# Kernel optimization log

Measured on AMD Instinct MI355X. Metric: run time of the kernel, lower is better.

## Reference

```python
import jax, jax.numpy as jnp
import numpy as np

N = 50000      # nodes
E = 800000     # edges (before self-loops)
IN = 128       # in_channels
HID = 16       # hidden_channels
HEADS = 8
OUT = 16       # out_channels
NEG_SLOPE = 0.2
BN_EPS = 1e-5
LN_EPS = 1e-5


def setup_inputs() -> dict:
    key = jax.random.key(0)
    ks = jax.random.split(key, 16)
    s = 0.05
    inp = {
        "x": jax.random.normal(ks[0], (N, IN), jnp.float32),
        "edge_index": jax.random.randint(ks[1], (2, E), 0, N, jnp.int64),
        # conv1 (in=IN, out=HID, heads=HEADS, concat=True)
        "Wl1": jax.random.normal(ks[2], (HEADS * HID, IN), jnp.float32) * s,
        "bl1": jnp.zeros((HEADS * HID,), jnp.float32),
        "Wr1": jax.random.normal(ks[3], (HEADS * HID, IN), jnp.float32) * s,
        "br1": jnp.zeros((HEADS * HID,), jnp.float32),
        "att1": jax.random.normal(ks[4], (HEADS, HID), jnp.float32) * s,
        "bias1": jnp.zeros((HEADS * HID,), jnp.float32),
        # batchnorm (eval mode, running stats)
        "bn_w": jnp.ones((HEADS * HID,), jnp.float32),
        "bn_b": jnp.zeros((HEADS * HID,), jnp.float32),
        "bn_rm": jnp.zeros((HEADS * HID,), jnp.float32),
        "bn_rv": jnp.ones((HEADS * HID,), jnp.float32),
        # conv2 (in=HEADS*HID, out=OUT, heads=HEADS, concat=False)
        "Wl2": jax.random.normal(ks[5], (HEADS * OUT, HEADS * HID), jnp.float32) * s,
        "bl2": jnp.zeros((HEADS * OUT,), jnp.float32),
        "Wr2": jax.random.normal(ks[6], (HEADS * OUT, HEADS * HID), jnp.float32) * s,
        "br2": jnp.zeros((HEADS * OUT,), jnp.float32),
        "att2": jax.random.normal(ks[7], (HEADS, OUT), jnp.float32) * s,
        "bias2": jnp.zeros((OUT,), jnp.float32),
        # skip + layernorm
        "Wskip": jax.random.normal(ks[8], (OUT, IN), jnp.float32) * s,
        "ln_w": jnp.ones((OUT,), jnp.float32),
        "ln_b": jnp.zeros((OUT,), jnp.float32),
    }
    return inp


def _gatv2(x, src, dst, Wl, bl, Wr, br, att, bias, heads, ch, concat):
    """PyG GATv2Conv (share_weights=False), eval mode (no dropout)."""
    n = x.shape[0]
    xl = (x @ Wl.T + bl).reshape(n, heads, ch)   # source transform
    xr = (x @ Wr.T + br).reshape(n, heads, ch)   # target transform
    # edge-wise attention score
    e = jax.nn.leaky_relu(xl[src] + xr[dst], NEG_SLOPE)          # [E',H,C]
    score = jnp.einsum('ehc,hc->eh', e, att)                      # [E',H]
    # segment softmax over incoming edges per destination node
    smax = jax.ops.segment_max(score, dst, num_segments=n)
    ex = jnp.exp(score - smax[dst])
    denom = jax.ops.segment_sum(ex, dst, num_segments=n)
    alpha = ex / denom[dst]                                       # [E',H]
    out = jax.ops.segment_sum(alpha[:, :, None] * xl[src], dst, num_segments=n)
    if concat:
        out = out.reshape(n, heads * ch)
    else:
        out = out.mean(axis=1)
    return out + bias


def reference(x, edge_index, Wl1, bl1, Wr1, br1, att1, bias1,
              bn_w, bn_b, bn_rm, bn_rv,
              Wl2, bl2, Wr2, br2, att2, bias2,
              Wskip, ln_w, ln_b):
    n = x.shape[0]
    loops = jnp.arange(n, dtype=edge_index.dtype)
    src = jnp.concatenate([edge_index[0], loops])
    dst = jnp.concatenate([edge_index[1], loops])

    x_res = x @ Wskip.T                                            # [N,OUT]

    h = _gatv2(x, src, dst, Wl1, bl1, Wr1, br1, att1, bias1, HEADS, HID, True)
    # BatchNorm1d in eval mode
    h = (h - bn_rm) * jax.lax.rsqrt(bn_rv + BN_EPS) * bn_w + bn_b
    h = jax.nn.elu(h)

    h = _gatv2(h, src, dst, Wl2, bl2, Wr2, br2, att2, bias2, HEADS, OUT, False)

    y = h + x_res
    mu = y.mean(axis=-1, keepdims=True)
    var = ((y - mu) ** 2).mean(axis=-1, keepdims=True)
    return (y - mu) * jax.lax.rsqrt(var + LN_EPS) * ln_w + ln_b
```

## Files before the change

kernel.cpp:

```cpp
#include <hip/hip_runtime.h>

#define NEG_SLOPE 0.2f
#define BN_EPS 1e-5f
#define LN_EPS 1e-5f

#if __has_builtin(__builtin_amdgcn_exp2f)
#define EXP2F(x) __builtin_amdgcn_exp2f(x)
#else
#define EXP2F(x) exp2f(x)
#endif

typedef __bf16 bf16_t;
typedef bf16_t bf16x8 __attribute__((ext_vector_type(8)));
typedef float floatx4 __attribute__((ext_vector_type(4)));

__device__ __forceinline__ unsigned short f2bf(float f) {
  unsigned u = __float_as_uint(f);
  u += 0x7FFFu + ((u >> 16) & 1u);
  return (unsigned short)(u >> 16);
}
__device__ __forceinline__ float bf_lo(unsigned u) { return __uint_as_float(u << 16); }
__device__ __forceinline__ float bf_hi(unsigned u) { return __uint_as_float(u & 0xFFFF0000u); }

__global__ void cvt_all(const float* __restrict__ x,
                        const float* __restrict__ wl1, const float* __restrict__ wr1,
                        const float* __restrict__ wl2, const float* __restrict__ wr2,
                        const float* __restrict__ wsk,
                        const float* __restrict__ bias1,
                        const float* __restrict__ bn_w, const float* __restrict__ bn_b,
                        const float* __restrict__ bn_rm, const float* __restrict__ bn_rv,
                        const int* __restrict__ ei, int E,
                        unsigned short* __restrict__ xbf,
                        unsigned short* __restrict__ wcat1,
                        unsigned short* __restrict__ wcat2,
                        int* __restrict__ deg8, unsigned short* __restrict__ rpos,
                        float* __restrict__ bnS, float* __restrict__ bnT,
                        int n4x, int N) {
  const int W4 = 128 * 128 / 4;
  const int S4 = 16 * 128 / 4;
  int i = blockIdx.x * blockDim.x + threadIdx.x;
  const float* src;
  unsigned short* dst;
  int j;
  if (i < n4x) { src = x; dst = xbf; j = i; }
  else {
    j = i - n4x;
    if (j < W4)               { src = wl1; dst = wcat1; }
    else if (j < 2 * W4)      { src = wr1; dst = wcat1 + 128 * 128; j -= W4; }
    else if (j < 3 * W4)      { src = wl2; dst = wcat2; j -= 2 * W4; }
    else if (j < 4 * W4)      { src = wr2; dst = wcat2 + 128 * 128; j -= 3 * W4; }
    else if (j < 4 * W4 + S4) { src = wsk; dst = wcat1 + 256 * 128; j -= 4 * W4; }
    else {
      j -= 4 * W4 + S4;
      if (j < 32) {
        for (int t = j * 4; t < j * 4 + 4; ++t) {
          float S = bn_w[t] * rsqrtf(bn_rv[t] + BN_EPS);
          bnS[t] = S;
          bnT[t] = (bias1[t] - bn_rm[t]) * S + bn_b[t];
        }
      } else {
        int e = j - 32;
        if (e < E) {
          int d = ei[E + e];
          int c = (int)(blockIdx.x & 7);
          rpos[e] = (unsigned short)atomicAdd(&deg8[(size_t)c * N + d], 1);
        }
      }
      return;
    }
  }
  float4 v = ((const float4*)src)[j];
  ushort4 o;
  o.x = f2bf(v.x); o.y = f2bf(v.y); o.z = f2bf(v.z); o.w = f2bf(v.w);
  ((ushort4*)dst)[j] = o;
}

__global__ __launch_bounds__(1024)
void csr_scan(const int* __restrict__ deg8, int* __restrict__ meta,
              int* __restrict__ cbase8, int* bsum, int N) {
  __shared__ int wsum[16];
  __shared__ int sh_base;
  int b = blockIdx.x;
  int tid = threadIdx.x;
  int lane = tid & 63, wid = tid >> 6;
  int i0 = b * 4096 + tid * 4;

  int4 v[8];
#pragma unroll
  for (int c = 0; c < 8; ++c) {
    const int* p = deg8 + (size_t)c * N;
    v[c] = make_int4(0, 0, 0, 0);
    if (i0 + 3 < N) v[c] = *(const int4*)(p + i0);
    else if (i0 < N) {
      v[c].x = p[i0];
      if (i0 + 1 < N) v[c].y = p[i0 + 1];
      if (i0 + 2 < N) v[c].z = p[i0 + 2];
    }
  }
  int4 run = make_int4(0, 0, 0, 0);
#pragma unroll
  for (int c = 0; c < 8; ++c) {
    int4 t = v[c];
    v[c] = run;
    run.x += t.x; run.y += t.y; run.z += t.z; run.w += t.w;
  }
  int g1 = (run.x + 1) & ~1, g2 = (run.y + 1) & ~1, g3 = (run.z + 1) & ~1, g4 = (run.w + 1) & ~1;
  int s1 = g1, s2 = s1 + g2, s3 = s2 + g3, s4 = s3 + g4;
  int s = s4;
#pragma unroll
  for (int d = 1; d < 64; d <<= 1) { int t = __shfl_up(s, d, 64); if (lane >= d) s += t; }
  if (lane == 63) wsum[wid] = s;
  __syncthreads();
  if (tid < 16) {
    int ws = wsum[tid];
#pragma unroll
    for (int d = 1; d < 16; d <<= 1) { int t = __shfl_up(ws, d, 16); if (tid >= d) ws += t; }
    wsum[tid] = ws;
  }
  __syncthreads();
  if (tid == 0) {
    __hip_atomic_store(&bsum[b], wsum[15] + 1, __ATOMIC_RELEASE, __HIP_MEMORY_SCOPE_AGENT);
    int base = 0;
    for (int j = 0; j < b; ++j) {
      int x;
      do { x = __hip_atomic_load(&bsum[j], __ATOMIC_ACQUIRE, __HIP_MEMORY_SCOPE_AGENT); } while (x == 0);
      base += x - 1;
    }
    sh_base = base;
  }
  __syncthreads();
  int off = sh_base + (wid ? wsum[wid - 1] : 0) + (s - s4);
  int st[4] = {off, off + s1, off + s2, off + s3};
  int tv[4] = {run.x, run.y, run.z, run.w};
#pragma unroll
  for (int k = 0; k < 4; ++k)
    if (i0 + k < N) ((int2*)meta)[i0 + k] = make_int2(st[k], tv[k]);
#pragma unroll
  for (int c = 0; c < 8; ++c) {
    int* p = cbase8 + (size_t)c * N;
    if (i0 + 3 < N) {
      *(int4*)(p + i0) = make_int4(st[0] + v[c].x, st[1] + v[c].y, st[2] + v[c].z, st[3] + v[c].w);
    } else if (i0 < N) {
      p[i0] = st[0] + v[c].x;
      if (i0 + 1 < N) p[i0 + 1] = st[1] + v[c].y;
      if (i0 + 2 < N) p[i0 + 2] = st[2] + v[c].z;
    }
  }
}

__global__ void scatter_edges(const int* __restrict__ ei, int E, int ebase,
                              const int* __restrict__ cbase8,
                              const unsigned short* __restrict__ rpos,
                              unsigned short* __restrict__ csr, int N) {
  int e = blockIdx.x * blockDim.x + threadIdx.x;
  if (e < E) {
    int d = ei[E + e];
    int c = ((ebase + e) >> 8) & 7;
    csr[cbase8[(size_t)c * N + d] + (int)rpos[e]] = (unsigned short)ei[e];
  }
}

template <bool MIXED>
__global__ __launch_bounds__(256)
void gemm_bf16_mfma(const unsigned short* __restrict__ A, const unsigned short* __restrict__ B,
                    const float* __restrict__ bias0, const float* __restrict__ bias1,
                    unsigned short* __restrict__ Cbf, float* __restrict__ Cf,
                    int M, int pstrips) {
  int wave = (int)((blockIdx.x * blockDim.x + threadIdx.x) >> 6);
  int lane = threadIdx.x & 63;
  int mtiles = (M + 31) >> 5;
  if (wave >= mtiles * pstrips) return;
  int mt = wave % mtiles, ps = wave / mtiles;
  int r = lane & 15, quad = lane >> 4;

  const unsigned short* Abase = A + (size_t)(mt * 32 + r) * 128 + quad * 8;
  bf16x8 a0[4], a1[4];
#pragma unroll
  for (int k = 0; k < 4; ++k) {
    a0[k] = *(const bf16x8*)(Abase + 32 * k);
    a1[k] = *(const bf16x8*)(Abase + 16 * 128 + 32 * k);
  }

  int row0 = mt * 32 + quad * 4;
  const int Ptot = MIXED ? 272 : 256;
#pragma unroll
  for (int pp = 0; pp < 4; ++pp) {
    int p0 = ps * 64 + pp * 16;
    if (p0 >= Ptot) break;
    const unsigned short* Bbase = B + (size_t)(p0 + r) * 128 + quad * 8;
    bf16x8 b[4];
#pragma unroll
    for (int k = 0; k < 4; ++k) b[k] = *(const bf16x8*)(Bbase + 32 * k);
    floatx4 acc0 = {0.f, 0.f, 0.f, 0.f};
    floatx4 acc1 = {0.f, 0.f, 0.f, 0.f};
#pragma unroll
    for (int k = 0; k < 4; ++k) {
      acc0 = __builtin_amdgcn_mfma_f32_16x16x32_bf16(a0[k], b[k], acc0, 0, 0, 0);
      acc1 = __builtin_amdgcn_mfma_f32_16x16x32_bf16(a1[k], b[k], acc1, 0, 0, 0);
    }
    int col = p0 + r;
    if (MIXED && col >= 256) {
#pragma unroll
      for (int i = 0; i < 4; ++i) {
        if (row0 + i < M)      Cf[(size_t)(row0 + i) * 16 + (col - 256)] = acc0[i];
        if (row0 + 16 + i < M) Cf[(size_t)(row0 + 16 + i) * 16 + (col - 256)] = acc1[i];
      }
    } else {
      float bs = (col < 128) ? bias0[col] : bias1[col - 128];
#pragma unroll
      for (int i = 0; i < 4; ++i) {
        if (row0 + i < M)      Cbf[(size_t)(row0 + i) * 256 + col] = f2bf(acc0[i] + bs);
        if (row0 + 16 + i < M) Cbf[(size_t)(row0 + 16 + i) * 256 + col] = f2bf(acc1[i] + bs);
      }
    }
  }
}

template <int LAYER>
__global__ __launch_bounds__(256)
void gat_agg(const unsigned int* __restrict__ xlr,
             const int* __restrict__ meta,
             const unsigned short* __restrict__ csr,
             const float* __restrict__ att,
             const float* __restrict__ p0, const float* __restrict__ p1,
             const float* __restrict__ p2, const float* __restrict__ p3,
             void* __restrict__ outp, int n, int nwaves) {
  int lane = threadIdx.x & 63;
  int gw = (int)((blockIdx.x * blockDim.x + threadIdx.x) >> 6);
  int half = lane >> 5, sl = lane & 31;
  float4 at = ((const float4*)att)[sl];
  const float SC = 0.6f * 1.44269504f;
  float a0 = SC * at.x, a1 = SC * at.y, a2 = SC * at.z, a3 = SC * at.w;

  for (int dst = gw; dst < n; dst += nwaves) {
    int dsts = __builtin_amdgcn_readfirstlane(dst);
    int2 m = *(const int2*)(meta + 2 * (size_t)dsts);
    int beg = __builtin_amdgcn_readfirstlane(m.x);
    int dg  = __builtin_amdgcn_readfirstlane(m.y);
    const unsigned* cp = (const unsigned*)csr + (beg >> 1);

    uint2 ur = *(const uint2*)(xlr + (size_t)dsts * 128 + 64 + sl * 2);
    float xr0 = bf_lo(ur.x), xr1 = bf_hi(ur.x), xr2 = bf_lo(ur.y), xr3 = bf_hi(ur.y);
    float lA = 0.f, lB = 0.f;
    float cA0 = 0.f, cA1 = 0.f, cA2 = 0.f, cA3 = 0.f;
    float cB0 = 0.f, cB1 = 0.f, cB2 = 0.f, cB3 = 0.f;

    auto body = [&](uint2 u, float vm, bool useB, bool masked) {
      float x0 = bf_lo(u.x), x1 = bf_hi(u.x), x2 = bf_lo(u.y), x3 = bf_hi(u.y);
      float e0 = x0 + xr0, e1 = x1 + xr1, e2 = x2 + xr2, e3 = x3 + xr3;
      float sc = fmaf(fmaf(fabsf(e0), 0.66666667f, e0), a0,
                 fmaf(fmaf(fabsf(e1), 0.66666667f, e1), a1,
                 fmaf(fmaf(fabsf(e2), 0.66666667f, e2), a2,
                      fmaf(fabsf(e3), 0.66666667f, e3) * a3)));
      sc += __shfl_xor(sc, 1);
      sc += __shfl_xor(sc, 2);
      float pw = EXP2F(sc);
      if (masked) pw *= vm;
      if (useB) {
        lB += pw;
        cB0 = fmaf(pw, x0, cB0); cB1 = fmaf(pw, x1, cB1);
        cB2 = fmaf(pw, x2, cB2); cB3 = fmaf(pw, x3, cB3);
      } else {
        lA += pw;
        cA0 = fmaf(pw, x0, cA0); cA1 = fmaf(pw, x1, cA1);
        cA2 = fmaf(pw, x2, cA2); cA3 = fmaf(pw, x3, cA3);
      }
    };

    int npm = dg >> 1;
    int p = 0;
    int npm8 = npm & ~7;
    for (; p < npm8; p += 8) {
      uint2 u[8];
#pragma unroll
      for (int k = 0; k < 8; ++k) {
        unsigned pr = cp[p + k];
        int s = half ? (int)(pr >> 16) : (int)(pr & 0xFFFFu);
        u[k] = *(const uint2*)(xlr + ((size_t)s << 7) + sl * 2);
      }
#pragma unroll
      for (int k = 0; k < 8; ++k) body(u[k], 1.f, k & 1, false);
    }
    if (npm - p >= 4) {
      uint2 u[4];
#pragma unroll
      for (int k = 0; k < 4; ++k) {
        unsigned pr = cp[p + k];
        int s = half ? (int)(pr >> 16) : (int)(pr & 0xFFFFu);
        u[k] = *(const uint2*)(xlr + ((size_t)s << 7) + sl * 2);
      }
#pragma unroll
      for (int k = 0; k < 4; ++k) body(u[k], 1.f, k & 1, false);
      p += 4;
    }
    {
      int tot = dg + 1;
      uint2 u[4];
      float vm[4];
#pragma unroll
      for (int k = 0; k < 4; ++k) {
        unsigned pr = cp[p + k];
        int e0 = 2 * (p + k), e1 = e0 + 1;
        int sA = (e0 < dg) ? (int)(pr & 0xFFFFu) : dsts;
        int sB = (e1 < dg) ? (int)(pr >> 16) : dsts;
        float mA = (e0 < tot) ? 1.f : 0.f;
        float mB = (e1 < tot) ? 1.f : 0.f;
        int s = half ? sB : sA;
        vm[k] = half ? mB : mA;
        u[k] = *(const uint2*)(xlr + ((size_t)s << 7) + sl * 2);
      }
#pragma unroll
      for (int k = 0; k < 4; ++k) body(u[k], vm[k], k & 1, true);
    }

    float l = lA + lB;
    float c0 = cA0 + cB0, c1 = cA1 + cB1, c2 = cA2 + cB2, c3 = cA3 + cB3;
    l  += __shfl_xor(l, 32);
    c0 += __shfl_xor(c0, 32); c1 += __shfl_xor(c1, 32);
    c2 += __shfl_xor(c2, 32); c3 += __shfl_xor(c3, 32);
    float inv = 1.f / l;

    if (LAYER == 1) {
      float4 S = ((const float4*)p0)[sl];
      float4 T = ((const float4*)p1)[sl];
      float o0 = fmaf(c0 * inv, S.x, T.x);
      float o1 = fmaf(c1 * inv, S.y, T.y);
      float o2 = fmaf(c2 * inv, S.z, T.z);
      float o3 = fmaf(c3 * inv, S.w, T.w);
      o0 = (o0 > 0.f) ? o0 : (__expf(o0) - 1.f);
      o1 = (o1 > 0.f) ? o1 : (__expf(o1) - 1.f);
      o2 = (o2 > 0.f) ? o2 : (__expf(o2) - 1.f);
      o3 = (o3 > 0.f) ? o3 : (__expf(o3) - 1.f);
      if (half == 0) {
        uint2 o;
        o.x = ((unsigned)f2bf(o1) << 16) | f2bf(o0);
        o.y = ((unsigned)f2bf(o3) << 16) | f2bf(o2);
        ((uint2*)outp)[(size_t)dst * 32 + sl] = o;
      }
    } else {
      float y0 = c0 * inv, y1 = c1 * inv, y2 = c2 * inv, y3 = c3 * inv;
#pragma unroll
      for (int d = 4; d <= 16; d <<= 1) {
        y0 += __shfl_xor(y0, d); y1 += __shfl_xor(y1, d);
        y2 += __shfl_xor(y2, d); y3 += __shfl_xor(y3, d);
      }
      int chh = (sl & 3) * 4;
      float4 b2 = *(const float4*)(p1 + chh);
      float4 xs = *(const float4*)(p0 + (size_t)dst * 16 + chh);
      y0 = y0 * 0.125f + b2.x + xs.x;
      y1 = y1 * 0.125f + b2.y + xs.y;
      y2 = y2 * 0.125f + b2.z + xs.z;
      y3 = y3 * 0.125f + b2.w + xs.w;
      float t = (y0 + y1) + (y2 + y3);
      t += __shfl_xor(t, 1); t += __shfl_xor(t, 2);
      float mu = t * (1.f / 16.f);
      float d0 = y0 - mu, d1 = y1 - mu, d2 = y2 - mu, d3 = y3 - mu;
      float v = (d0 * d0 + d1 * d1) + (d2 * d2 + d3 * d3);
      v += __shfl_xor(v, 1); v += __shfl_xor(v, 2);
      float istd = rsqrtf(v * (1.f / 16.f) + LN_EPS);
      float4 lw = *(const float4*)(p2 + chh);
      float4 lb = *(const float4*)(p3 + chh);
      if (lane < 4) {
        float4 o;
        o.x = d0 * istd * lw.x + lb.x;
        o.y = d1 * istd * lw.y + lb.y;
        o.z = d2 * istd * lw.z + lb.z;
        o.w = d3 * istd * lw.w + lb.w;
        *(float4*)((float*)outp + (size_t)dst * 16 + chh) = o;
      }
    }
  }
}

extern "C" void kernel_launch(void* const* d_in, const int* in_sizes, int n_in,
                              void* d_out, int out_size, void* d_ws, size_t ws_size,
                              hipStream_t stream) {
  const float* x     = (const float*)d_in[0];
  const int*   ei    = (const int*)d_in[1];
  const float* Wl1   = (const float*)d_in[2];
  const float* bl1   = (const float*)d_in[3];
  const float* Wr1   = (const float*)d_in[4];
  const float* br1   = (const float*)d_in[5];
  const float* att1  = (const float*)d_in[6];
  const float* bias1 = (const float*)d_in[7];
  const float* bn_w  = (const float*)d_in[8];
  const float* bn_b  = (const float*)d_in[9];
  const float* bn_rm = (const float*)d_in[10];
  const float* bn_rv = (const float*)d_in[11];
  const float* Wl2   = (const float*)d_in[12];
  const float* bl2   = (const float*)d_in[13];
  const float* Wr2   = (const float*)d_in[14];
  const float* br2   = (const float*)d_in[15];
  const float* att2  = (const float*)d_in[16];
  const float* bias2 = (const float*)d_in[17];
  const float* Wskip = (const float*)d_in[18];
  const float* ln_w  = (const float*)d_in[19];
  const float* ln_b  = (const float*)d_in[20];

  const int N = in_sizes[0] / 128;
  const int E = in_sizes[1] / 2;

  char* w = (char*)d_ws;
  size_t off = 0;
  auto alloc = [&](size_t bytes) -> void* {
    void* p = (void*)(w + off);
    off += (bytes + 255) & ~(size_t)255;
    return p;
  };
  unsigned short* xbf    = (unsigned short*)alloc((size_t)N * 128 * 2);
  unsigned short* wcat1  = (unsigned short*)alloc(272 * 128 * 2);
  unsigned short* wcat2  = (unsigned short*)alloc(256 * 128 * 2);
  unsigned int*   xlr    = (unsigned int*)alloc((size_t)N * 128 * 4);
  float*          xres   = (float*)alloc((size_t)N * 16 * 4);
  unsigned short* hbf    = (unsigned short*)alloc((size_t)N * 128 * 2);
  float*          bnS    = (float*)alloc(128 * 4);
  float*          bnT    = (float*)alloc(128 * 4);
  int*            deg8   = (int*)alloc((size_t)8 * N * 4);
  int*            bsum   = (int*)alloc(64 * 4);
  int*            cbase8 = (int*)alloc((size_t)8 * N * 4);
  int*            meta   = (int*)alloc((size_t)2 * N * 4);
  unsigned short* rpos   = (unsigned short*)alloc((size_t)E * 2);
  unsigned short* csr    = (unsigned short*)alloc((size_t)(E + N) * 2 + 256);

  const int n4x = (N * 128) / 4;
  const int W4 = 128 * 128 / 4, S4 = 16 * 128 / 4;
  const int ebase = n4x + 4 * W4 + S4 + 32;
  const int nb = (N + 4095) / 4096;

  hipMemsetAsync(deg8, 0, (size_t)8 * N * 4 + 256 + 64 * 4, stream);
  {
    int tot = ebase + E;
    cvt_all<<<(tot + 255) / 256, 256, 0, stream>>>(
        x, Wl1, Wr1, Wl2, Wr2, Wskip, bias1, bn_w, bn_b, bn_rm, bn_rv, ei, E,
        xbf, wcat1, wcat2, deg8, rpos, bnS, bnT, n4x, N);
  }

  csr_scan<<<nb, 1024, 0, stream>>>(deg8, meta, cbase8, bsum, N);
  scatter_edges<<<(E + 255) / 256, 256, 0, stream>>>(ei, E, ebase, cbase8, rpos, csr, N);

  {
    int mtiles = (N + 31) >> 5;
    int waves = mtiles * 5;
    gemm_bf16_mfma<true><<<(waves + 3) / 4, 256, 0, stream>>>(
        xbf, wcat1, bl1, br1, (unsigned short*)xlr, xres, N, 5);
  }

  {
    int blocks = 2048, nwaves = blocks * 4;
    gat_agg<1><<<blocks, 256, 0, stream>>>(xlr, meta, csr, att1,
                                           bnS, bnT, nullptr, nullptr, (void*)hbf, N, nwaves);
  }

  {
    int mtiles = (N + 31) >> 5;
    int waves = mtiles * 4;
    gemm_bf16_mfma<false><<<(waves + 3) / 4, 256, 0, stream>>>(
        hbf, wcat2, bl2, br2, (unsigned short*)xlr, nullptr, N, 4);
  }

  {
    int blocks = 2048, nwaves = blocks * 4;
    gat_agg<2><<<blocks, 256, 0, stream>>>(xlr, meta, csr, att2,
                                           xres, bias2, ln_w, ln_b, d_out, N, nwaves);
  }
}
```

Measured before the change: 302.8 us.

## Reuse A fragments across strips in GEMM and prefetch next node metadata in aggregation

```diff
diff --git a/kernel.cpp b/kernel.cpp
--- a/kernel.cpp
+++ b/kernel.cpp
@@ -166,11 +166,11 @@
                     const float* __restrict__ bias0, const float* __restrict__ bias1,
                     unsigned short* __restrict__ Cbf, float* __restrict__ Cf,
                     int M, int pstrips) {
-  int wave = (int)((blockIdx.x * blockDim.x + threadIdx.x) >> 6);
+  int wv = (int)((blockIdx.x * blockDim.x + threadIdx.x) >> 6);
   int lane = threadIdx.x & 63;
   int mtiles = (M + 31) >> 5;
-  if (wave >= mtiles * pstrips) return;
-  int mt = wave % mtiles, ps = wave / mtiles;
+  if (wv >= mtiles * 2) return;
+  int mt = wv >> 1, sub = wv & 1;
   int r = lane & 15, quad = lane >> 4;
 
   const unsigned short* Abase = A + (size_t)(mt * 32 + r) * 128 + quad * 8;
@@ -183,34 +183,36 @@
 
   int row0 = mt * 32 + quad * 4;
   const int Ptot = MIXED ? 272 : 256;
-#pragma unroll
-  for (int pp = 0; pp < 4; ++pp) {
-    int p0 = ps * 64 + pp * 16;
-    if (p0 >= Ptot) break;
-    const unsigned short* Bbase = B + (size_t)(p0 + r) * 128 + quad * 8;
-    bf16x8 b[4];
-#pragma unroll
-    for (int k = 0; k < 4; ++k) b[k] = *(const bf16x8*)(Bbase + 32 * k);
-    floatx4 acc0 = {0.f, 0.f, 0.f, 0.f};
-    floatx4 acc1 = {0.f, 0.f, 0.f, 0.f};
-#pragma unroll
-    for (int k = 0; k < 4; ++k) {
-      acc0 = __builtin_amdgcn_mfma_f32_16x16x32_bf16(a0[k], b[k], acc0, 0, 0, 0);
-      acc1 = __builtin_amdgcn_mfma_f32_16x16x32_bf16(a1[k], b[k], acc1, 0, 0, 0);
-    }
-    int col = p0 + r;
-    if (MIXED && col >= 256) {
-#pragma unroll
-      for (int i = 0; i < 4; ++i) {
-        if (row0 + i < M)      Cf[(size_t)(row0 + i) * 16 + (col - 256)] = acc0[i];
-        if (row0 + 16 + i < M) Cf[(size_t)(row0 + 16 + i) * 16 + (col - 256)] = acc1[i];
-      }
-    } else {
-      float bs = (col < 128) ? bias0[col] : bias1[col - 128];
-#pragma unroll
-      for (int i = 0; i < 4; ++i) {
-        if (row0 + i < M)      Cbf[(size_t)(row0 + i) * 256 + col] = f2bf(acc0[i] + bs);
-        if (row0 + 16 + i < M) Cbf[(size_t)(row0 + 16 + i) * 256 + col] = f2bf(acc1[i] + bs);
+  for (int ps = sub; ps < pstrips; ps += 2) {
+#pragma unroll
+    for (int pp = 0; pp < 4; ++pp) {
+      int p0 = ps * 64 + pp * 16;
+      if (p0 >= Ptot) break;
+      const unsigned short* Bbase = B + (size_t)(p0 + r) * 128 + quad * 8;
+      bf16x8 b[4];
+#pragma unroll
+      for (int k = 0; k < 4; ++k) b[k] = *(const bf16x8*)(Bbase + 32 * k);
+      floatx4 acc0 = {0.f, 0.f, 0.f, 0.f};
+      floatx4 acc1 = {0.f, 0.f, 0.f, 0.f};
+#pragma unroll
+      for (int k = 0; k < 4; ++k) {
+        acc0 = __builtin_amdgcn_mfma_f32_16x16x32_bf16(a0[k], b[k], acc0, 0, 0, 0);
+        acc1 = __builtin_amdgcn_mfma_f32_16x16x32_bf16(a1[k], b[k], acc1, 0, 0, 0);
+      }
+      int col = p0 + r;
+      if (MIXED && col >= 256) {
+#pragma unroll
+        for (int i = 0; i < 4; ++i) {
+          if (row0 + i < M)      Cf[(size_t)(row0 + i) * 16 + (col - 256)] = acc0[i];
+          if (row0 + 16 + i < M) Cf[(size_t)(row0 + 16 + i) * 16 + (col - 256)] = acc1[i];
+        }
+      } else {
+        float bs = (col < 128) ? bias0[col] : bias1[col - 128];
+#pragma unroll
+        for (int i = 0; i < 4; ++i) {
+          if (row0 + i < M)      Cbf[(size_t)(row0 + i) * 256 + col] = f2bf(acc0[i] + bs);
+          if (row0 + 16 + i < M) Cbf[(size_t)(row0 + 16 + i) * 256 + col] = f2bf(acc1[i] + bs);
+        }
       }
     }
   }
@@ -228,22 +230,47 @@
   int lane = threadIdx.x & 63;
   int gw = (int)((blockIdx.x * blockDim.x + threadIdx.x) >> 6);
   int half = lane >> 5, sl = lane & 31;
+  const char* __restrict__ xb = (const char*)xlr;
+  const unsigned slOff = (unsigned)(sl << 3);
+  const int hshift = half << 4;
   float4 at = ((const float4*)att)[sl];
   const float SC = 0.6f * 1.44269504f;
   float a0 = SC * at.x, a1 = SC * at.y, a2 = SC * at.z, a3 = SC * at.w;
 
-  for (int dst = gw; dst < n; dst += nwaves) {
+  int dst = gw;
+  int2 m = make_int2(0, 0);
+  uint2 ur = make_uint2(0u, 0u);
+  if (dst < n) {
+    int ds0 = __builtin_amdgcn_readfirstlane(dst);
+    m = *(const int2*)(meta + 2 * (size_t)ds0);
+    ur = *(const uint2*)(xb + (((unsigned)ds0 << 9) + 256u + slOff));
+  }
+
+  while (dst < n) {
     int dsts = __builtin_amdgcn_readfirstlane(dst);
-    int2 m = *(const int2*)(meta + 2 * (size_t)dsts);
     int beg = __builtin_amdgcn_readfirstlane(m.x);
     int dg  = __builtin_amdgcn_readfirstlane(m.y);
     const unsigned* cp = (const unsigned*)csr + (beg >> 1);
 
-    uint2 ur = *(const uint2*)(xlr + (size_t)dsts * 128 + 64 + sl * 2);
     float xr0 = bf_lo(ur.x), xr1 = bf_hi(ur.x), xr2 = bf_lo(ur.y), xr3 = bf_hi(ur.y);
+
+    int nxt = dst + nwaves;
+    int2 m_n = make_int2(0, 0);
+    uint2 ur_n = make_uint2(0u, 0u);
+    if (nxt < n) {
+      int dsn = __builtin_amdgcn_readfirstlane(nxt);
+      m_n = *(const int2*)(meta + 2 * (size_t)dsn);
+      ur_n = *(const uint2*)(xb + (((unsigned)dsn << 9) + 256u + slOff));
+    }
+
     float lA = 0.f, lB = 0.f;
     float cA0 = 0.f, cA1 = 0.f, cA2 = 0.f, cA3 = 0.f;
     float cB0 = 0.f, cB1 = 0.f, cB2 = 0.f, cB3 = 0.f;
+
+    auto gat = [&](unsigned pr) -> uint2 {
+      unsigned s = (pr >> hshift) & 0xFFFFu;
+      return *(const uint2*)(xb + ((s << 9) + slOff));
+    };
 
     auto body = [&](uint2 u, float vm, bool useB, bool masked) {
       float x0 = bf_lo(u.x), x1 = bf_hi(u.x), x2 = bf_lo(u.y), x3 = bf_hi(u.y);
@@ -273,44 +300,56 @@
     for (; p < npm8; p += 8) {
       uint2 u[8];
 #pragma unroll
-      for (int k = 0; k < 8; ++k) {
-        unsigned pr = cp[p + k];
-        int s = half ? (int)(pr >> 16) : (int)(pr & 0xFFFFu);
-        u[k] = *(const uint2*)(xlr + ((size_t)s << 7) + sl * 2);
-      }
+      for (int k = 0; k < 8; ++k) u[k] = gat(cp[p + k]);
 #pragma unroll
       for (int k = 0; k < 8; ++k) body(u[k], 1.f, k & 1, false);
     }
     if (npm - p >= 4) {
       uint2 u[4];
 #pragma unroll
-      for (int k = 0; k < 4; ++k) {
-        unsigned pr = cp[p + k];
-        int s = half ? (int)(pr >> 16) : (int)(pr & 0xFFFFu);
-        u[k] = *(const uint2*)(xlr + ((size_t)s << 7) + sl * 2);
-      }
+      for (int k = 0; k < 4; ++k) u[k] = gat(cp[p + k]);
 #pragma unroll
       for (int k = 0; k < 4; ++k) body(u[k], 1.f, k & 1, false);
       p += 4;
     }
     {
       int tot = dg + 1;
-      uint2 u[4];
-      float vm[4];
-#pragma unroll
-      for (int k = 0; k < 4; ++k) {
-        unsigned pr = cp[p + k];
-        int e0 = 2 * (p + k), e1 = e0 + 1;
-        int sA = (e0 < dg) ? (int)(pr & 0xFFFFu) : dsts;
-        int sB = (e1 < dg) ? (int)(pr >> 16) : dsts;
-        float mA = (e0 < tot) ? 1.f : 0.f;
-        float mB = (e1 < tot) ? 1.f : 0.f;
-        int s = half ? sB : sA;
-        vm[k] = half ? mB : mA;
-        u[k] = *(const uint2*)(xlr + ((size_t)s << 7) + sl * 2);
-      }
-#pragma unroll
-      for (int k = 0; k < 4; ++k) body(u[k], vm[k], k & 1, true);
+      int need = tot - 2 * p;
+      if (need > 4) {
+        uint2 u[4];
+        float vm[4];
+#pragma unroll
+        for (int k = 0; k < 4; ++k) {
+          unsigned pr = cp[p + k];
+          int e0 = 2 * (p + k), e1 = e0 + 1;
+          int sA = (e0 < dg) ? (int)(pr & 0xFFFFu) : dsts;
+          int sB = (e1 < dg) ? (int)(pr >> 16) : dsts;
+          float mA = (e0 < tot) ? 1.f : 0.f;
+          float mB = (e1 < tot) ? 1.f : 0.f;
+          unsigned s = (unsigned)(half ? sB : sA);
+          vm[k] = half ? mB : mA;
+          u[k] = *(const uint2*)(xb + ((s << 9) + slOff));
+        }
+#pragma unroll
+        for (int k = 0; k < 4; ++k) body(u[k], vm[k], k & 1, true);
+      } else {
+        uint2 u[2];
+        float vm[2];
+#pragma unroll
+        for (int k = 0; k < 2; ++k) {
+          unsigned pr = cp[p + k];
+          int e0 = 2 * (p + k), e1 = e0 + 1;
+          int sA = (e0 < dg) ? (int)(pr & 0xFFFFu) : dsts;
+          int sB = (e1 < dg) ? (int)(pr >> 16) : dsts;
+          float mA = (e0 < tot) ? 1.f : 0.f;
+          float mB = (e1 < tot) ? 1.f : 0.f;
+          unsigned s = (unsigned)(half ? sB : sA);
+          vm[k] = half ? mB : mA;
+          u[k] = *(const uint2*)(xb + ((s << 9) + slOff));
+        }
+#pragma unroll
+        for (int k = 0; k < 2; ++k) body(u[k], vm[k], k & 1, true);
+      }
     }
 
     float l = lA + lB;
@@ -369,6 +408,10 @@
         *(float4*)((float*)outp + (size_t)dst * 16 + chh) = o;
       }
     }
+
+    m = m_n;
+    ur = ur_n;
+    dst = nxt;
   }
 }
 
@@ -440,7 +483,7 @@
 
   {
     int mtiles = (N + 31) >> 5;
-    int waves = mtiles * 5;
+    int waves = mtiles * 2;
     gemm_bf16_mfma<true><<<(waves + 3) / 4, 256, 0, stream>>>(
         xbf, wcat1, bl1, br1, (unsigned short*)xlr, xres, N, 5);
   }
@@ -453,7 +496,7 @@
 
   {
     int mtiles = (N + 31) >> 5;
-    int waves = mtiles * 4;
+    int waves = mtiles * 2;
     gemm_bf16_mfma<false><<<(waves + 3) / 4, 256, 0, stream>>>(
         hbf, wcat2, bl2, br2, (unsigned short*)xlr, nullptr, N, 4);
   }
```

Result: no change. 306.1 us (+1.1%).

## Add atomic work-stealing scheduler to GAT aggregation and reuse A tiles across GEMM strips

Applied to the files above, without the earlier changes.

```diff
diff --git a/kernel.cpp b/kernel.cpp
--- a/kernel.cpp
+++ b/kernel.cpp
@@ -166,11 +166,11 @@
                     const float* __restrict__ bias0, const float* __restrict__ bias1,
                     unsigned short* __restrict__ Cbf, float* __restrict__ Cf,
                     int M, int pstrips) {
-  int wave = (int)((blockIdx.x * blockDim.x + threadIdx.x) >> 6);
+  int wv = (int)((blockIdx.x * blockDim.x + threadIdx.x) >> 6);
   int lane = threadIdx.x & 63;
   int mtiles = (M + 31) >> 5;
-  if (wave >= mtiles * pstrips) return;
-  int mt = wave % mtiles, ps = wave / mtiles;
+  if (wv >= mtiles * 2) return;
+  int mt = wv >> 1, sub = wv & 1;
   int r = lane & 15, quad = lane >> 4;
 
   const unsigned short* Abase = A + (size_t)(mt * 32 + r) * 128 + quad * 8;
@@ -183,34 +183,36 @@
 
   int row0 = mt * 32 + quad * 4;
   const int Ptot = MIXED ? 272 : 256;
-#pragma unroll
-  for (int pp = 0; pp < 4; ++pp) {
-    int p0 = ps * 64 + pp * 16;
-    if (p0 >= Ptot) break;
-    const unsigned short* Bbase = B + (size_t)(p0 + r) * 128 + quad * 8;
-    bf16x8 b[4];
-#pragma unroll
-    for (int k = 0; k < 4; ++k) b[k] = *(const bf16x8*)(Bbase + 32 * k);
-    floatx4 acc0 = {0.f, 0.f, 0.f, 0.f};
-    floatx4 acc1 = {0.f, 0.f, 0.f, 0.f};
-#pragma unroll
-    for (int k = 0; k < 4; ++k) {
-      acc0 = __builtin_amdgcn_mfma_f32_16x16x32_bf16(a0[k], b[k], acc0, 0, 0, 0);
-      acc1 = __builtin_amdgcn_mfma_f32_16x16x32_bf16(a1[k], b[k], acc1, 0, 0, 0);
-    }
-    int col = p0 + r;
-    if (MIXED && col >= 256) {
-#pragma unroll
-      for (int i = 0; i < 4; ++i) {
-        if (row0 + i < M)      Cf[(size_t)(row0 + i) * 16 + (col - 256)] = acc0[i];
-        if (row0 + 16 + i < M) Cf[(size_t)(row0 + 16 + i) * 16 + (col - 256)] = acc1[i];
-      }
-    } else {
-      float bs = (col < 128) ? bias0[col] : bias1[col - 128];
-#pragma unroll
-      for (int i = 0; i < 4; ++i) {
-        if (row0 + i < M)      Cbf[(size_t)(row0 + i) * 256 + col] = f2bf(acc0[i] + bs);
-        if (row0 + 16 + i < M) Cbf[(size_t)(row0 + 16 + i) * 256 + col] = f2bf(acc1[i] + bs);
+  for (int ps = sub; ps < pstrips; ps += 2) {
+#pragma unroll
+    for (int pp = 0; pp < 4; ++pp) {
+      int p0 = ps * 64 + pp * 16;
+      if (p0 >= Ptot) break;
+      const unsigned short* Bbase = B + (size_t)(p0 + r) * 128 + quad * 8;
+      bf16x8 b[4];
+#pragma unroll
+      for (int k = 0; k < 4; ++k) b[k] = *(const bf16x8*)(Bbase + 32 * k);
+      floatx4 acc0 = {0.f, 0.f, 0.f, 0.f};
+      floatx4 acc1 = {0.f, 0.f, 0.f, 0.f};
+#pragma unroll
+      for (int k = 0; k < 4; ++k) {
+        acc0 = __builtin_amdgcn_mfma_f32_16x16x32_bf16(a0[k], b[k], acc0, 0, 0, 0);
+        acc1 = __builtin_amdgcn_mfma_f32_16x16x32_bf16(a1[k], b[k], acc1, 0, 0, 0);
+      }
+      int col = p0 + r;
+      if (MIXED && col >= 256) {
+#pragma unroll
+        for (int i = 0; i < 4; ++i) {
+          if (row0 + i < M)      Cf[(size_t)(row0 + i) * 16 + (col - 256)] = acc0[i];
+          if (row0 + 16 + i < M) Cf[(size_t)(row0 + 16 + i) * 16 + (col - 256)] = acc1[i];
+        }
+      } else {
+        float bs = (col < 128) ? bias0[col] : bias1[col - 128];
+#pragma unroll
+        for (int i = 0; i < 4; ++i) {
+          if (row0 + i < M)      Cbf[(size_t)(row0 + i) * 256 + col] = f2bf(acc0[i] + bs);
+          if (row0 + 16 + i < M) Cbf[(size_t)(row0 + 16 + i) * 256 + col] = f2bf(acc1[i] + bs);
+        }
       }
     }
   }
@@ -224,26 +226,40 @@
              const float* __restrict__ att,
              const float* __restrict__ p0, const float* __restrict__ p1,
              const float* __restrict__ p2, const float* __restrict__ p3,
-             void* __restrict__ outp, int n, int nwaves) {
+             void* __restrict__ outp, int n,
+             int* __restrict__ cursor, int pp) {
   int lane = threadIdx.x & 63;
-  int gw = (int)((blockIdx.x * blockDim.x + threadIdx.x) >> 6);
   int half = lane >> 5, sl = lane & 31;
+  const char* __restrict__ xb = (const char*)xlr;
+  const unsigned slOff = (unsigned)(sl << 3);
+  const int hshift = half << 4;
   float4 at = ((const float4*)att)[sl];
   const float SC = 0.6f * 1.44269504f;
   float a0 = SC * at.x, a1 = SC * at.y, a2 = SC * at.z, a3 = SC * at.w;
 
-  for (int dst = gw; dst < n; dst += nwaves) {
-    int dsts = __builtin_amdgcn_readfirstlane(dst);
+  const int g = (int)(blockIdx.x & 7);
+  const int base = g * pp;
+  const int lim = min(pp, n - base);
+  const int wig = (int)(blockIdx.x >> 3) * (int)(blockDim.x >> 6) + (int)(threadIdx.x >> 6);
+  const int seed = (int)(gridDim.x >> 3) * (int)(blockDim.x >> 6) * 4;
+
+  auto process = [&](int dstv) {
+    int dsts = __builtin_amdgcn_readfirstlane(dstv);
     int2 m = *(const int2*)(meta + 2 * (size_t)dsts);
     int beg = __builtin_amdgcn_readfirstlane(m.x);
     int dg  = __builtin_amdgcn_readfirstlane(m.y);
     const unsigned* cp = (const unsigned*)csr + (beg >> 1);
-
-    uint2 ur = *(const uint2*)(xlr + (size_t)dsts * 128 + 64 + sl * 2);
+    uint2 ur = *(const uint2*)(xb + (((unsigned)dsts << 9) + 256u + slOff));
     float xr0 = bf_lo(ur.x), xr1 = bf_hi(ur.x), xr2 = bf_lo(ur.y), xr3 = bf_hi(ur.y);
+
     float lA = 0.f, lB = 0.f;
     float cA0 = 0.f, cA1 = 0.f, cA2 = 0.f, cA3 = 0.f;
     float cB0 = 0.f, cB1 = 0.f, cB2 = 0.f, cB3 = 0.f;
+
+    auto gat = [&](unsigned pr) -> uint2 {
+      unsigned s = (pr >> hshift) & 0xFFFFu;
+      return *(const uint2*)(xb + ((s << 9) + slOff));
+    };
 
     auto body = [&](uint2 u, float vm, bool useB, bool masked) {
       float x0 = bf_lo(u.x), x1 = bf_hi(u.x), x2 = bf_lo(u.y), x3 = bf_hi(u.y);
@@ -273,22 +289,14 @@
     for (; p < npm8; p += 8) {
       uint2 u[8];
 #pragma unroll
-      for (int k = 0; k < 8; ++k) {
-        unsigned pr = cp[p + k];
-        int s = half ? (int)(pr >> 16) : (int)(pr & 0xFFFFu);
-        u[k] = *(const uint2*)(xlr + ((size_t)s << 7) + sl * 2);
-      }
+      for (int k = 0; k < 8; ++k) u[k] = gat(cp[p + k]);
 #pragma unroll
       for (int k = 0; k < 8; ++k) body(u[k], 1.f, k & 1, false);
     }
     if (npm - p >= 4) {
       uint2 u[4];
 #pragma unroll
-      for (int k = 0; k < 4; ++k) {
-        unsigned pr = cp[p + k];
-        int s = half ? (int)(pr >> 16) : (int)(pr & 0xFFFFu);
-        u[k] = *(const uint2*)(xlr + ((size_t)s << 7) + sl * 2);
-      }
+      for (int k = 0; k < 4; ++k) u[k] = gat(cp[p + k]);
 #pragma unroll
       for (int k = 0; k < 4; ++k) body(u[k], 1.f, k & 1, false);
       p += 4;
@@ -305,9 +313,9 @@
         int sB = (e1 < dg) ? (int)(pr >> 16) : dsts;
         float mA = (e0 < tot) ? 1.f : 0.f;
         float mB = (e1 < tot) ? 1.f : 0.f;
-        int s = half ? sB : sA;
+        unsigned s = (unsigned)(half ? sB : sA);
         vm[k] = half ? mB : mA;
-        u[k] = *(const uint2*)(xlr + ((size_t)s << 7) + sl * 2);
+        u[k] = *(const uint2*)(xb + ((s << 9) + slOff));
       }
 #pragma unroll
       for (int k = 0; k < 4; ++k) body(u[k], vm[k], k & 1, true);
@@ -335,7 +343,7 @@
         uint2 o;
         o.x = ((unsigned)f2bf(o1) << 16) | f2bf(o0);
         o.y = ((unsigned)f2bf(o3) << 16) | f2bf(o2);
-        ((uint2*)outp)[(size_t)dst * 32 + sl] = o;
+        ((uint2*)outp)[(size_t)dsts * 32 + sl] = o;
       }
     } else {
       float y0 = c0 * inv, y1 = c1 * inv, y2 = c2 * inv, y3 = c3 * inv;
@@ -346,7 +354,7 @@
       }
       int chh = (sl & 3) * 4;
       float4 b2 = *(const float4*)(p1 + chh);
-      float4 xs = *(const float4*)(p0 + (size_t)dst * 16 + chh);
+      float4 xs = *(const float4*)(p0 + (size_t)dsts * 16 + chh);
       y0 = y0 * 0.125f + b2.x + xs.x;
       y1 = y1 * 0.125f + b2.y + xs.y;
       y2 = y2 * 0.125f + b2.z + xs.z;
@@ -366,9 +374,24 @@
         o.y = d1 * istd * lw.y + lb.y;
         o.z = d2 * istd * lw.z + lb.z;
         o.w = d3 * istd * lw.w + lb.w;
-        *(float4*)((float*)outp + (size_t)dst * 16 + chh) = o;
-      }
-    }
+        *(float4*)((float*)outp + (size_t)dsts * 16 + chh) = o;
+      }
+    }
+  };
+
+  {
+    int s0 = wig * 4;
+    int e0 = min(s0 + 4, lim);
+    for (int ii = s0; ii < e0; ++ii) process(base + ii);
+  }
+  for (;;) {
+    int t = 0;
+    if (lane == 0) t = atomicAdd(cursor + g, 4);
+    t = __shfl(t, 0);
+    int s0 = seed + t;
+    if (s0 >= lim) break;
+    int e0 = min(s0 + 4, lim);
+    for (int ii = s0; ii < e0; ++ii) process(base + ii);
   }
 }
 
@@ -417,6 +440,8 @@
   float*          bnT    = (float*)alloc(128 * 4);
   int*            deg8   = (int*)alloc((size_t)8 * N * 4);
   int*            bsum   = (int*)alloc(64 * 4);
+  int*            cur1   = (int*)alloc(8 * 4);
+  int*            cur2   = (int*)alloc(8 * 4);
   int*            cbase8 = (int*)alloc((size_t)8 * N * 4);
   int*            meta   = (int*)alloc((size_t)2 * N * 4);
   unsigned short* rpos   = (unsigned short*)alloc((size_t)E * 2);
@@ -427,7 +452,7 @@
   const int ebase = n4x + 4 * W4 + S4 + 32;
   const int nb = (N + 4095) / 4096;
 
-  hipMemsetAsync(deg8, 0, (size_t)8 * N * 4 + 256 + 64 * 4, stream);
+  hipMemsetAsync(deg8, 0, (size_t)8 * N * 4 + 3 * 256, stream);
   {
     int tot = ebase + E;
     cvt_all<<<(tot + 255) / 256, 256, 0, stream>>>(
@@ -440,27 +465,23 @@
 
   {
     int mtiles = (N + 31) >> 5;
-    int waves = mtiles * 5;
+    int waves = mtiles * 2;
     gemm_bf16_mfma<true><<<(waves + 3) / 4, 256, 0, stream>>>(
         xbf, wcat1, bl1, br1, (unsigned short*)xlr, xres, N, 5);
   }
 
-  {
-    int blocks = 2048, nwaves = blocks * 4;
-    gat_agg<1><<<blocks, 256, 0, stream>>>(xlr, meta, csr, att1,
-                                           bnS, bnT, nullptr, nullptr, (void*)hbf, N, nwaves);
-  }
+  const int pp = (N + 7) / 8;
+
+  gat_agg<1><<<2048, 256, 0, stream>>>(xlr, meta, csr, att1,
+                                       bnS, bnT, nullptr, nullptr, (void*)hbf, N, cur1, pp);
 
   {
     int mtiles = (N + 31) >> 5;
-    int waves = mtiles * 4;
+    int waves = mtiles * 2;
     gemm_bf16_mfma<false><<<(waves + 3) / 4, 256, 0, stream>>>(
         hbf, wcat2, bl2, br2, (unsigned short*)xlr, nullptr, N, 4);
   }
 
-  {
-    int blocks = 2048, nwaves = blocks * 4;
-    gat_agg<2><<<blocks, 256, 0, stream>>>(xlr, meta, csr, att2,
-                                           xres, bias2, ln_w, ln_b, d_out, N, nwaves);
-  }
-}
+  gat_agg<2><<<2048, 256, 0, stream>>>(xlr, meta, csr, att2,
+                                       xres, bias2, ln_w, ln_b, d_out, N, cur2, pp);
+}
```

New measurement: 539.4 us. 1.78x slower.
